# Optimization experiments

Measured on AMD Instinct MI355X. Metric: run time of the kernel, lower is better.

## Reference

```python
import jax, jax.numpy as jnp
import numpy as np

EPS = 1e-6
N_SRC = 100000
N_TAR = 100000
N = N_SRC + N_TAR
DIM = 128
E = 600000
NEG_SLOPE = 0.01  # torch leaky_relu default


def setup_inputs() -> dict:
    key = jax.random.key(0)
    ks = jax.random.split(key, 8)
    x_src = jax.random.normal(ks[0], (N_SRC, DIM), dtype=jnp.float32)
    x_tar = jax.random.normal(ks[1], (N_TAR, DIM), dtype=jnp.float32)
    edge_index = jax.random.randint(ks[2], (2, E), 0, N, dtype=jnp.int64)
    edge_weight = jax.random.uniform(ks[3], (E,), dtype=jnp.float32)
    W_gcn = jax.random.normal(ks[4], (DIM, DIM), dtype=jnp.float32) / np.sqrt(DIM)
    b_gcn = jax.random.normal(ks[5], (DIM,), dtype=jnp.float32) * 0.01
    W_fnn = jax.random.normal(ks[6], (DIM, DIM), dtype=jnp.float32) / np.sqrt(DIM)
    b_fnn = jax.random.normal(ks[7], (DIM,), dtype=jnp.float32) * 0.01
    return dict(x_src=x_src, x_tar=x_tar, edge_index=edge_index,
                edge_weight=edge_weight, W_gcn=W_gcn, b_gcn=b_gcn,
                W_fnn=W_fnn, b_fnn=b_fnn)


def _gcn_conv(x, edge_index, edge_weight, W, b):
    # PyG GCNConv with add_self_loops=True, symmetric normalization.
    row = jnp.concatenate([edge_index[0], jnp.arange(N, dtype=edge_index.dtype)])
    col = jnp.concatenate([edge_index[1], jnp.arange(N, dtype=edge_index.dtype)])
    w = jnp.concatenate([edge_weight, jnp.ones((N,), dtype=edge_weight.dtype)])
    deg = jax.ops.segment_sum(w, col, num_segments=N)
    dinv = jnp.where(deg > 0, jax.lax.rsqrt(deg), 0.0)
    norm = dinv[row] * w * dinv[col]                 # [E+N]
    h = x @ W                                        # [N, D]
    msg = norm[:, None] * h[row]                     # gather + scale
    out = jnp.zeros_like(h).at[col].add(msg)         # scatter-add to targets
    return out + b


def _node_norm(x):
    mean = jnp.mean(x, axis=1, keepdims=True)
    var = jnp.mean((x - mean) ** 2, axis=1, keepdims=True)  # unbiased=False
    return (x - mean) / jnp.sqrt(var + EPS)


def reference(x_src, x_tar, edge_index, edge_weight, W_gcn, b_gcn, W_fnn, b_fnn):
    x = jnp.concatenate([x_src, x_tar], axis=0)      # [N, D]
    # route == 'MIX': GNN branch + FNN branch on the skip copy
    g = _gcn_conv(x, edge_index, edge_weight, W_gcn, b_gcn)
    f = jax.nn.leaky_relu(x @ W_fnn + b_fnn, NEG_SLOPE)  # dropout = identity (eval)
    x = g + f
    x = _node_norm(x)
    x = jax.nn.leaky_relu(x, NEG_SLOPE)
    return x[:N_SRC, :], x[N_SRC:, :]
```

## Files before the change

### kernel.cpp

```cpp
#include <hip/hip_runtime.h>
#include <hip/hip_bf16.h>
#include <cstddef>
#include <cstdint>

#define DIM 128
#define SCAN_CHUNK 2048

typedef __attribute__((ext_vector_type(8))) short short8v;
typedef __attribute__((ext_vector_type(4))) float f32x4;

__device__ __forceinline__ float leaky(float v) {
    return v > 0.0f ? v : 0.01f * v;
}

__device__ __forceinline__ unsigned short f2bf(float f) {
    unsigned u = __builtin_bit_cast(unsigned, f);
    u += 0x7FFF + ((u >> 16) & 1);
    return (unsigned short)(u >> 16);
}

__device__ __forceinline__ unsigned cvt_pk_bf16(float a, float b) {
    unsigned r;
    asm("v_cvt_pk_bf16_f32 %0, %1, %2" : "=v"(r) : "v"(a), "v"(b));
    return r;
}

__device__ __forceinline__ float bf2f_hi(unsigned p) {
    return __builtin_bit_cast(float, p & 0xFFFF0000u);
}
__device__ __forceinline__ float bf2f_lo(unsigned p) {
    return __builtin_bit_cast(float, p << 16);
}

__device__ __forceinline__ void gload_lds16(const float* g, float* lds) {
    __builtin_amdgcn_global_load_lds(
        (const __attribute__((address_space(1))) unsigned int*)g,
        (__attribute__((address_space(3))) unsigned int*)lds, 16, 0, 0);
}

__global__ __launch_bounds__(256)
void init_kernel(const float* __restrict__ Wg, const float* __restrict__ Wf,
                 unsigned short* __restrict__ WgT, unsigned short* __restrict__ WfT,
                 int* __restrict__ cnt, int N) {
    int t = blockIdx.x * 256 + threadIdx.x;
    if (t < N) cnt[t] = 0;
    if (t < 128 * 128) {
        int col = t >> 7, k = t & 127;
        WgT[col * 128 + k] = f2bf(Wg[k * 128 + col]);
        WfT[col * 128 + k] = f2bf(Wf[k * 128 + col]);
    }
}

__global__ __launch_bounds__(256)
void hist_kernel(const int* __restrict__ col, int* __restrict__ cnt, int E) {
    int e = blockIdx.x * blockDim.x + threadIdx.x;
    if (e < E) atomicAdd(&cnt[col[e]], 1);
}

__global__ __launch_bounds__(256)
void scan_block_sums(const int* __restrict__ cnt, int* __restrict__ bsum, int N) {
    __shared__ int sdata[4];
    int base = blockIdx.x * SCAN_CHUNK;
    int s = 0;
    for (int k = threadIdx.x; k < SCAN_CHUNK; k += 256) {
        int idx = base + k;
        s += (idx < N) ? cnt[idx] : 0;
    }
#pragma unroll
    for (int m = 1; m < 64; m <<= 1) s += __shfl_xor(s, m, 64);
    if ((threadIdx.x & 63) == 0) sdata[threadIdx.x >> 6] = s;
    __syncthreads();
    if (threadIdx.x == 0)
        bsum[blockIdx.x] = sdata[0] + sdata[1] + sdata[2] + sdata[3];
}

__global__ __launch_bounds__(128)
void scan_bsum_kernel(int* __restrict__ bsum, int nb) {
    __shared__ int wtot[2];
    int t = threadIdx.x;
    int lane = t & 63;
    int orig = (t < nb) ? bsum[t] : 0;
    int v = orig;
#pragma unroll
    for (int m = 1; m < 64; m <<= 1) {
        int u = __shfl_up(v, m, 64);
        if (lane >= m) v += u;
    }
    if (lane == 63) wtot[t >> 6] = v;
    __syncthreads();
    if (t >= 64) v += wtot[0];
    if (t < nb) bsum[t] = v - orig;
}

__global__ __launch_bounds__(256)
void scan_write_kernel(int* __restrict__ cnt, const int* __restrict__ bsum,
                       int* __restrict__ off, int N) {
    __shared__ int wsum[4];
    int t = threadIdx.x;
    int base = blockIdx.x * SCAN_CHUNK + t * 8;
    int vals[8];
    int local = 0;
#pragma unroll
    for (int k = 0; k < 8; ++k) {
        int idx = base + k;
        int c = (idx < N) ? cnt[idx] : 0;
        vals[k] = local;
        local += c;
    }
    int tsum = local;
    int lane = t & 63;
    int v = tsum;
#pragma unroll
    for (int m = 1; m < 64; m <<= 1) {
        int u = __shfl_up(v, m, 64);
        if (lane >= m) v += u;
    }
    if (lane == 63) wsum[t >> 6] = v;
    __syncthreads();
    int woff = 0;
    for (int i = 0; i < (t >> 6); ++i) woff += wsum[i];
    int texcl = (v - tsum) + woff + bsum[blockIdx.x];
#pragma unroll
    for (int k = 0; k < 8; ++k) {
        int idx = base + k;
        int o = texcl + vals[k];
        if (idx <= N) off[idx] = o;
    }
    __syncthreads();
#pragma unroll
    for (int k = 0; k < 8; ++k) {
        int idx = base + k;
        int o = texcl + vals[k];
        if (idx < N) cnt[idx] = o;
    }
}

__global__ __launch_bounds__(256)
void reorder_kernel(const int* __restrict__ row, const int* __restrict__ col,
                    const float* __restrict__ w, int* __restrict__ cursor,
                    int2* __restrict__ edgeRW, int E) {
    int e = blockIdx.x * blockDim.x + threadIdx.x;
    if (e < E) {
        int c = col[e];
        int pos = atomicAdd(&cursor[c], 1);
        edgeRW[pos] = make_int2(row[e], __builtin_bit_cast(int, w[e]));
    }
}

__global__ __launch_bounds__(256)
void csr_dinv_kernel(const int* __restrict__ off, const int2* __restrict__ edgeRW,
                     float* __restrict__ dinv, int N) {
    int i = blockIdx.x * 256 + threadIdx.x;
    if (i >= N) return;
    int s = off[i], e = off[i + 1];
    float acc = 1.0f;
    for (int j = s; j < e; ++j)
        acc += __builtin_bit_cast(float, edgeRW[j].y);
    dinv[i] = rsqrtf(acc);
}

__global__ __launch_bounds__(512, 4)
void gemm_mfma_kernel(const float* __restrict__ x_src, const float* __restrict__ x_tar,
                      int n_src, int n_total, int ntiles,
                      const unsigned short* __restrict__ WgT,
                      const unsigned short* __restrict__ WfT,
                      const float* __restrict__ bg, const float* __restrict__ bf,
                      const float* __restrict__ dinv,
                      unsigned short* __restrict__ hsb,
                      unsigned short* __restrict__ accb)
{
    __shared__ float Ash[2][64 * 128];

    const int t    = threadIdx.x;
    const int lane = t & 63;
    const int wv   = t >> 6;
    const int h    = wv >> 2;
    const int q    = wv & 3;
    const int lr   = lane & 15;
    const int lk   = lane >> 4;
    const int nb   = gridDim.x;

    short8v wg[4][2], wf[4][2];
#pragma unroll
    for (int ks = 0; ks < 4; ++ks)
#pragma unroll
        for (int nf = 0; nf < 2; ++nf) {
            int col = q * 32 + nf * 16 + lr;
            const size_t bo = (size_t)col * 128 + ks * 32 + lk * 8;
            wg[ks][nf] = *(const short8v*)(WgT + bo);
            wf[ks][nf] = *(const short8v*)(WfT + bo);
        }

    auto stage = [&](int tl, int buf) {
#pragma unroll
        for (int s = 0; s < 4; ++s) {
            int id  = s * 512 + t;
            int row = id >> 5;
            int cs  = id & 31;
            int c   = cs ^ (row & 15);
            int rg  = tl * 64 + row;
            if (rg >= n_total) rg = n_total - 1;
            const float* xr = (rg < n_src) ? x_src + (size_t)rg * DIM
                                           : x_tar + (size_t)(rg - n_src) * DIM;
            gload_lds16(xr + c * 4, &Ash[buf][(size_t)(s * 512 + wv * 64) * 4]);
        }
    };

    int tile = blockIdx.x;
    if (tile < ntiles) stage(tile, 0);
    int cur = 0;

    for (; tile < ntiles; tile += nb) {
        __syncthreads();
        if (tile + nb < ntiles) stage(tile + nb, cur ^ 1);

        f32x4 accg[2][2], accf[2][2];
#pragma unroll
        for (int i = 0; i < 2; ++i)
#pragma unroll
            for (int j = 0; j < 2; ++j) {
                accg[i][j] = (f32x4)0.0f;
                accf[i][j] = (f32x4)0.0f;
            }

#pragma unroll
        for (int ks = 0; ks < 4; ++ks) {
            short8v xf[2];
#pragma unroll
            for (int mf = 0; mf < 2; ++mf) {
                int row = h * 32 + mf * 16 + lr;
                int c0  = ks * 8 + lk * 2;
                float4 q0 = *(const float4*)&Ash[cur][(size_t)(row * 32 + ( c0      ^ (row & 15))) * 4];
                float4 q1 = *(const float4*)&Ash[cur][(size_t)(row * 32 + ((c0 + 1) ^ (row & 15))) * 4];
                union { short8v v; unsigned u[4]; } cv;
                cv.u[0] = cvt_pk_bf16(q0.x, q0.y);
                cv.u[1] = cvt_pk_bf16(q0.z, q0.w);
                cv.u[2] = cvt_pk_bf16(q1.x, q1.y);
                cv.u[3] = cvt_pk_bf16(q1.z, q1.w);
                xf[mf] = cv.v;
            }
#pragma unroll
            for (int nf = 0; nf < 2; ++nf)
#pragma unroll
                for (int mf = 0; mf < 2; ++mf) {
                    accg[mf][nf] = __builtin_amdgcn_mfma_f32_16x16x32_bf16(wg[ks][nf], xf[mf], accg[mf][nf], 0, 0, 0);
                    accf[mf][nf] = __builtin_amdgcn_mfma_f32_16x16x32_bf16(wf[ks][nf], xf[mf], accf[mf][nf], 0, 0, 0);
                }
        }

#pragma unroll
        for (int mf = 0; mf < 2; ++mf) {
            int r = tile * 64 + h * 32 + mf * 16 + lr;
            const bool valid = (r < n_total);
            int rc = valid ? r : (n_total - 1);
            float dv = dinv[rc];
#pragma unroll
            for (int nf = 0; nf < 2; ++nf) {
                int c0 = q * 32 + nf * 16 + lk * 4;
                float4 bgv = *(const float4*)(bg + c0);
                float4 bfv = *(const float4*)(bf + c0);

                float hs0 = dv * accg[mf][nf][0];
                float hs1 = dv * accg[mf][nf][1];
                float hs2 = dv * accg[mf][nf][2];
                float hs3 = dv * accg[mf][nf][3];

                float o0 = leaky(accf[mf][nf][0] + bfv.x) + bgv.x + dv * hs0;
                float o1 = leaky(accf[mf][nf][1] + bfv.y) + bgv.y + dv * hs1;
                float o2 = leaky(accf[mf][nf][2] + bfv.z) + bgv.z + dv * hs2;
                float o3 = leaky(accf[mf][nf][3] + bfv.w) + bgv.w + dv * hs3;

                uint2 hp, op;
                hp.x = cvt_pk_bf16(hs0, hs1);
                hp.y = cvt_pk_bf16(hs2, hs3);
                op.x = cvt_pk_bf16(o0, o1);
                op.y = cvt_pk_bf16(o2, o3);

                if (valid) {
                    *(uint2*)(hsb  + (size_t)r * DIM + c0) = hp;
                    *(uint2*)(accb + (size_t)r * DIM + c0) = op;
                }
            }
        }
        cur ^= 1;
    }
}

__global__ __launch_bounds__(256)
void gather_norm_kernel(const int* __restrict__ off, const int2* __restrict__ edgeRW,
                        const float* __restrict__ dinv,
                        const unsigned short* __restrict__ hsb,
                        const unsigned short* __restrict__ accb,
                        float* __restrict__ out, int n)
{
    const int wid  = threadIdx.x >> 6;
    const int lane = threadIdx.x & 63;
    const int sub  = lane >> 4;
    const int sl   = lane & 15;
    int i = (blockIdx.x * 4 + wid) * 4 + sub;
    if (i >= n) i = n - 1;

    const int start = off[i];
    const int degc  = off[i + 1] - start;

    int md = degc;
    md = max(md, __shfl_xor(md, 16, 64));
    md = max(md, __shfl_xor(md, 32, 64));

    float s[8];
#pragma unroll
    for (int k = 0; k < 8; ++k) s[k] = 0.0f;

    const unsigned short* gbase = hsb + (size_t)sl * 8;

    int   r0 = 0, r1 = 0;
    float w0 = 0.0f, w1 = 0.0f;
    if (0 < degc) { int2 m = edgeRW[start];     r0 = m.x; w0 = __builtin_bit_cast(float, m.y); }
    if (1 < degc) { int2 m = edgeRW[start + 1]; r1 = m.x; w1 = __builtin_bit_cast(float, m.y); }
    uint4 p0 = *(const uint4*)(gbase + (size_t)r0 * DIM);

    for (int t = 0; t < md; ++t) {
        uint4 p1 = p0;
        if (t + 1 < md)
            p1 = *(const uint4*)(gbase + (size_t)r1 * DIM);
        int r2 = 0; float w2 = 0.0f;
        if (t + 2 < md) {
            if (t + 2 < degc) {
                int2 m = edgeRW[start + t + 2];
                r2 = m.x; w2 = __builtin_bit_cast(float, m.y);
            }
        }
        s[0] += w0 * bf2f_lo(p0.x); s[1] += w0 * bf2f_hi(p0.x);
        s[2] += w0 * bf2f_lo(p0.y); s[3] += w0 * bf2f_hi(p0.y);
        s[4] += w0 * bf2f_lo(p0.z); s[5] += w0 * bf2f_hi(p0.z);
        s[6] += w0 * bf2f_lo(p0.w); s[7] += w0 * bf2f_hi(p0.w);
        p0 = p1;
        r0 = r1; w0 = w1;
        r1 = r2; w1 = w2;
    }

    const float dv = dinv[i];
    uint4 av = *(const uint4*)(accb + (size_t)i * DIM + sl * 8);
    float v[8];
    v[0] = bf2f_lo(av.x) + dv * s[0]; v[1] = bf2f_hi(av.x) + dv * s[1];
    v[2] = bf2f_lo(av.y) + dv * s[2]; v[3] = bf2f_hi(av.y) + dv * s[3];
    v[4] = bf2f_lo(av.z) + dv * s[4]; v[5] = bf2f_hi(av.z) + dv * s[5];
    v[6] = bf2f_lo(av.w) + dv * s[6]; v[7] = bf2f_hi(av.w) + dv * s[7];

    float sum = 0.0f;
#pragma unroll
    for (int k = 0; k < 8; ++k) sum += v[k];
#pragma unroll
    for (int m = 1; m < 16; m <<= 1) sum += __shfl_xor(sum, m, 64);
    const float mean = sum * (1.0f / 128.0f);

    float sq = 0.0f;
#pragma unroll
    for (int k = 0; k < 8; ++k) {
        v[k] -= mean;
        sq += v[k] * v[k];
    }
#pragma unroll
    for (int m = 1; m < 16; m <<= 1) sq += __shfl_xor(sq, m, 64);
    const float rstd = rsqrtf(sq * (1.0f / 128.0f) + 1e-6f);

    float4 o1, o2;
    o1.x = leaky(v[0] * rstd); o1.y = leaky(v[1] * rstd);
    o1.z = leaky(v[2] * rstd); o1.w = leaky(v[3] * rstd);
    o2.x = leaky(v[4] * rstd); o2.y = leaky(v[5] * rstd);
    o2.z = leaky(v[6] * rstd); o2.w = leaky(v[7] * rstd);
    float* op = out + (size_t)i * DIM + sl * 8;
    *(float4*)op       = o1;
    *(float4*)(op + 4) = o2;
}

extern "C" void kernel_launch(void* const* d_in, const int* in_sizes, int n_in,
                              void* d_out, int out_size, void* d_ws, size_t ws_size,
                              hipStream_t stream)
{
    const float* x_src = (const float*)d_in[0];
    const float* x_tar = (const float*)d_in[1];
    const int*   ei    = (const int*)d_in[2];
    const float* ew    = (const float*)d_in[3];
    const float* Wg    = (const float*)d_in[4];
    const float* bg    = (const float*)d_in[5];
    const float* Wf    = (const float*)d_in[6];
    const float* bf    = (const float*)d_in[7];

    const int n_src = in_sizes[0] / DIM;
    const int n_tar = in_sizes[1] / DIM;
    const int N     = n_src + n_tar;
    const int E     = in_sizes[3];

    const int* rowp = ei;
    const int* colp = ei + E;

    char* p = (char*)d_ws;
    float* dinv = (float*)p;  p += (size_t)N * 4;
    int*   cnt  = (int*)p;    p += (size_t)N * 4;
    int*   off  = (int*)p;    p += (size_t)(N + 1) * 4;
    int*   bsum = (int*)p;    p += 160 * 4;
    p = (char*)(((uintptr_t)p + 15) & ~(uintptr_t)15);
    int2*  edgeRW = (int2*)p; p += (size_t)E * 8;
    unsigned short* hsb  = (unsigned short*)p; p += (size_t)N * DIM * 2;
    unsigned short* accb = (unsigned short*)p; p += (size_t)N * DIM * 2;
    unsigned short* WgT  = (unsigned short*)p; p += 128 * 128 * 2;
    unsigned short* WfT  = (unsigned short*)p;

    const int NB = (N + 1 + SCAN_CHUNK - 1) / SCAN_CHUNK;

    init_kernel<<<(N + 255) / 256, 256, 0, stream>>>(Wg, Wf, WgT, WfT, cnt, N);

    hist_kernel<<<(E + 255) / 256, 256, 0, stream>>>(colp, cnt, E);

    scan_block_sums<<<NB, 256, 0, stream>>>(cnt, bsum, N);
    scan_bsum_kernel<<<1, 128, 0, stream>>>(bsum, NB);
    scan_write_kernel<<<NB, 256, 0, stream>>>(cnt, bsum, off, N);

    reorder_kernel<<<(E + 255) / 256, 256, 0, stream>>>(rowp, colp, ew, cnt,
                                                        edgeRW, E);

    csr_dinv_kernel<<<(N + 255) / 256, 256, 0, stream>>>(off, edgeRW, dinv, N);

    const int ntiles = (N + 63) / 64;
    gemm_mfma_kernel<<<512, 512, 0, stream>>>(
        x_src, x_tar, n_src, N, ntiles, WgT, WfT, bg, bf, dinv, hsb, accb);

    gather_norm_kernel<<<(N + 15) / 16, 256, 0, stream>>>(
        off, edgeRW, dinv, hsb, accb, (float*)d_out, N);
}
```

Baseline: 226.2 us.

## Deepen GEMM staging pipeline to four 32-row buffers with contiguous tile ranges

The fused dual-GEMM kernel now uses 32-row tiles with a four-slot LDS ring that keeps three tiles in flight, instead of a two-slot double buffer of 64-row tiles. Each block takes a contiguous range of tiles. It waits on hand-tuned vmcnt values rather than a full drain, so loads overlap compute more deeply. dinv values for the block's rows are preloaded into shared memory, and biases are hoisted out of the loop. The hand-counted vmcnt thresholds are fragile, and halving the tile height halves the MFMA work per barrier.

```diff
diff --git a/kernel.cpp b/kernel.cpp
--- a/kernel.cpp
+++ b/kernel.cpp
@@ -169,7 +169,8 @@
                       unsigned short* __restrict__ hsb,
                       unsigned short* __restrict__ accb)
 {
-    __shared__ float Ash[2][64 * 128];
+    __shared__ float Ash[4][32 * 128];
+    __shared__ float dinvS[448];
 
     const int t    = threadIdx.x;
     const int lane = t & 63;
@@ -178,7 +179,19 @@
     const int q    = wv & 3;
     const int lr   = lane & 15;
     const int lk   = lane >> 4;
-    const int nb   = gridDim.x;
+
+    const int nb  = gridDim.x;
+    const int K   = (ntiles + nb - 1) / nb;
+    const int t0  = blockIdx.x * K;
+    const int cnt = min(K, ntiles - t0);
+    if (cnt <= 0) return;
+
+    if (t < cnt * 32) {
+        int gi = t0 * 32 + t;
+        if (gi >= n_total) gi = n_total - 1;
+        dinvS[t] = dinv[gi];
+    }
+    asm volatile("s_waitcnt lgkmcnt(0)" ::: "memory");
 
     short8v wg[4][2], wf[4][2];
 #pragma unroll
@@ -190,15 +203,22 @@
             wg[ks][nf] = *(const short8v*)(WgT + bo);
             wf[ks][nf] = *(const short8v*)(WfT + bo);
         }
+    float4 bgv[2], bfv[2];
+#pragma unroll
+    for (int nf = 0; nf < 2; ++nf) {
+        int c0 = q * 32 + nf * 16 + lk * 4;
+        bgv[nf] = *(const float4*)(bg + c0);
+        bfv[nf] = *(const float4*)(bf + c0);
+    }
 
     auto stage = [&](int tl, int buf) {
 #pragma unroll
-        for (int s = 0; s < 4; ++s) {
+        for (int s = 0; s < 2; ++s) {
             int id  = s * 512 + t;
             int row = id >> 5;
             int cs  = id & 31;
             int c   = cs ^ (row & 15);
-            int rg  = tl * 64 + row;
+            int rg  = tl * 32 + row;
             if (rg >= n_total) rg = n_total - 1;
             const float* xr = (rg < n_src) ? x_src + (size_t)rg * DIM
                                            : x_tar + (size_t)(rg - n_src) * DIM;
@@ -206,83 +226,81 @@
         }
     };
 
-    int tile = blockIdx.x;
-    if (tile < ntiles) stage(tile, 0);
-    int cur = 0;
-
-    for (; tile < ntiles; tile += nb) {
-        __syncthreads();
-        if (tile + nb < ntiles) stage(tile + nb, cur ^ 1);
-
-        f32x4 accg[2][2], accf[2][2];
-#pragma unroll
-        for (int i = 0; i < 2; ++i)
-#pragma unroll
-            for (int j = 0; j < 2; ++j) {
-                accg[i][j] = (f32x4)0.0f;
-                accf[i][j] = (f32x4)0.0f;
+    stage(t0, 0);
+    if (1 < cnt) stage(t0 + 1, 1);
+    if (2 < cnt) stage(t0 + 2, 2);
+
+    const int xrow = h * 16 + lr;
+    const int xrs  = xrow & 15;
+
+    for (int it = 0; it < cnt; ++it) {
+        if (cnt >= 6) {
+            if (it == 0)              asm volatile("s_waitcnt vmcnt(4)"  ::: "memory");
+            else if (it == 1)         asm volatile("s_waitcnt vmcnt(8)"  ::: "memory");
+            else if (it == 2)         asm volatile("s_waitcnt vmcnt(12)" ::: "memory");
+            else if (it == cnt - 2)   asm volatile("s_waitcnt vmcnt(14)" ::: "memory");
+            else if (it == cnt - 1)   asm volatile("s_waitcnt vmcnt(12)" ::: "memory");
+            else                      asm volatile("s_waitcnt vmcnt(16)" ::: "memory");
+        } else {
+            asm volatile("s_waitcnt vmcnt(0)" ::: "memory");
+        }
+        __builtin_amdgcn_sched_barrier(0);
+        __builtin_amdgcn_s_barrier();
+        __builtin_amdgcn_sched_barrier(0);
+
+        if (it + 3 < cnt) stage(t0 + it + 3, (it + 3) & 3);
+
+        const int cur = it & 3;
+        f32x4 accg[2], accf[2];
+        accg[0] = (f32x4)0.0f; accg[1] = (f32x4)0.0f;
+        accf[0] = (f32x4)0.0f; accf[1] = (f32x4)0.0f;
+
+#pragma unroll
+        for (int ks = 0; ks < 4; ++ks) {
+            int c0 = ks * 8 + lk * 2;
+            float4 q0 = *(const float4*)&Ash[cur][(size_t)(xrow * 32 + ( c0      ^ xrs)) * 4];
+            float4 q1 = *(const float4*)&Ash[cur][(size_t)(xrow * 32 + ((c0 + 1) ^ xrs)) * 4];
+            union { short8v v; unsigned u[4]; } cv;
+            cv.u[0] = cvt_pk_bf16(q0.x, q0.y);
+            cv.u[1] = cvt_pk_bf16(q0.z, q0.w);
+            cv.u[2] = cvt_pk_bf16(q1.x, q1.y);
+            cv.u[3] = cvt_pk_bf16(q1.z, q1.w);
+#pragma unroll
+            for (int nf = 0; nf < 2; ++nf) {
+                accg[nf] = __builtin_amdgcn_mfma_f32_16x16x32_bf16(wg[ks][nf], cv.v, accg[nf], 0, 0, 0);
+                accf[nf] = __builtin_amdgcn_mfma_f32_16x16x32_bf16(wf[ks][nf], cv.v, accf[nf], 0, 0, 0);
             }
-
-#pragma unroll
-        for (int ks = 0; ks < 4; ++ks) {
-            short8v xf[2];
-#pragma unroll
-            for (int mf = 0; mf < 2; ++mf) {
-                int row = h * 32 + mf * 16 + lr;
-                int c0  = ks * 8 + lk * 2;
-                float4 q0 = *(const float4*)&Ash[cur][(size_t)(row * 32 + ( c0      ^ (row & 15))) * 4];
-                float4 q1 = *(const float4*)&Ash[cur][(size_t)(row * 32 + ((c0 + 1) ^ (row & 15))) * 4];
-                union { short8v v; unsigned u[4]; } cv;
-                cv.u[0] = cvt_pk_bf16(q0.x, q0.y);
-                cv.u[1] = cvt_pk_bf16(q0.z, q0.w);
-                cv.u[2] = cvt_pk_bf16(q1.x, q1.y);
-                cv.u[3] = cvt_pk_bf16(q1.z, q1.w);
-                xf[mf] = cv.v;
+        }
+
+        const int tile = t0 + it;
+        int r = tile * 32 + xrow;
+        const bool valid = (r < n_total);
+        float dv = dinvS[it * 32 + xrow];
+#pragma unroll
+        for (int nf = 0; nf < 2; ++nf) {
+            int c0 = q * 32 + nf * 16 + lk * 4;
+
+            float hs0 = dv * accg[nf][0];
+            float hs1 = dv * accg[nf][1];
+            float hs2 = dv * accg[nf][2];
+            float hs3 = dv * accg[nf][3];
+
+            float o0 = leaky(accf[nf][0] + bfv[nf].x) + bgv[nf].x + dv * hs0;
+            float o1 = leaky(accf[nf][1] + bfv[nf].y) + bgv[nf].y + dv * hs1;
+            float o2 = leaky(accf[nf][2] + bfv[nf].z) + bgv[nf].z + dv * hs2;
+            float o3 = leaky(accf[nf][3] + bfv[nf].w) + bgv[nf].w + dv * hs3;
+
+            uint2 hp, op;
+            hp.x = cvt_pk_bf16(hs0, hs1);
+            hp.y = cvt_pk_bf16(hs2, hs3);
+            op.x = cvt_pk_bf16(o0, o1);
+            op.y = cvt_pk_bf16(o2, o3);
+
+            if (valid) {
+                *(uint2*)(hsb  + (size_t)r * DIM + c0) = hp;
+                *(uint2*)(accb + (size_t)r * DIM + c0) = op;
             }
-#pragma unroll
-            for (int nf = 0; nf < 2; ++nf)
-#pragma unroll
-                for (int mf = 0; mf < 2; ++mf) {
-                    accg[mf][nf] = __builtin_amdgcn_mfma_f32_16x16x32_bf16(wg[ks][nf], xf[mf], accg[mf][nf], 0, 0, 0);
-                    accf[mf][nf] = __builtin_amdgcn_mfma_f32_16x16x32_bf16(wf[ks][nf], xf[mf], accf[mf][nf], 0, 0, 0);
-                }
-        }
-
-#pragma unroll
-        for (int mf = 0; mf < 2; ++mf) {
-            int r = tile * 64 + h * 32 + mf * 16 + lr;
-            const bool valid = (r < n_total);
-            int rc = valid ? r : (n_total - 1);
-            float dv = dinv[rc];
-#pragma unroll
-            for (int nf = 0; nf < 2; ++nf) {
-                int c0 = q * 32 + nf * 16 + lk * 4;
-                float4 bgv = *(const float4*)(bg + c0);
-                float4 bfv = *(const float4*)(bf + c0);
-
-                float hs0 = dv * accg[mf][nf][0];
-                float hs1 = dv * accg[mf][nf][1];
-                float hs2 = dv * accg[mf][nf][2];
-                float hs3 = dv * accg[mf][nf][3];
-
-                float o0 = leaky(accf[mf][nf][0] + bfv.x) + bgv.x + dv * hs0;
-                float o1 = leaky(accf[mf][nf][1] + bfv.y) + bgv.y + dv * hs1;
-                float o2 = leaky(accf[mf][nf][2] + bfv.z) + bgv.z + dv * hs2;
-                float o3 = leaky(accf[mf][nf][3] + bfv.w) + bgv.w + dv * hs3;
-
-                uint2 hp, op;
-                hp.x = cvt_pk_bf16(hs0, hs1);
-                hp.y = cvt_pk_bf16(hs2, hs3);
-                op.x = cvt_pk_bf16(o0, o1);
-                op.y = cvt_pk_bf16(o2, o3);
-
-                if (valid) {
-                    *(uint2*)(hsb  + (size_t)r * DIM + c0) = hp;
-                    *(uint2*)(accb + (size_t)r * DIM + c0) = op;
-                }
-            }
-        }
-        cur ^= 1;
+        }
     }
 }
 
@@ -422,7 +440,7 @@
 
     csr_dinv_kernel<<<(N + 255) / 256, 256, 0, stream>>>(off, edgeRW, dinv, N);
 
-    const int ntiles = (N + 63) / 64;
+    const int ntiles = (N + 31) / 32;
     gemm_mfma_kernel<<<512, 512, 0, stream>>>(
         x_src, x_tar, n_src, N, ntiles, WgT, WfT, bg, bf, dinv, hsb, accb);
 
```

Result: faster. 205.6 us (-9.1%).

## Replace LDS-staged persistent GEMM with direct-load one-tile-per-block GEMM

Applied to the files above, without the earlier changes.

Rewrites the dual-weight MFMA GEMM so each 256-thread block handles 32 rows and loads x straight from global memory into registers, dropping the double-buffered LDS staging, the persistent tile loop and its barriers. The weight column mapping is permuted so each lane owns 8 contiguous output columns, which allows 16-byte bf16 stores instead of 8-byte ones. This removes LDS traffic and synchronisation, at the cost of losing load/compute overlap and having each x row read by all four waves, with the repeat reads served from cache.

```diff
diff --git a/kernel.cpp b/kernel.cpp
--- a/kernel.cpp
+++ b/kernel.cpp
@@ -30,12 +30,6 @@
 }
 __device__ __forceinline__ float bf2f_lo(unsigned p) {
     return __builtin_bit_cast(float, p << 16);
-}
-
-__device__ __forceinline__ void gload_lds16(const float* g, float* lds) {
-    __builtin_amdgcn_global_load_lds(
-        (const __attribute__((address_space(1))) unsigned int*)g,
-        (__attribute__((address_space(3))) unsigned int*)lds, 16, 0, 0);
 }
 
 __global__ __launch_bounds__(256)
@@ -159,130 +153,107 @@
     dinv[i] = rsqrtf(acc);
 }
 
-__global__ __launch_bounds__(512, 4)
-void gemm_mfma_kernel(const float* __restrict__ x_src, const float* __restrict__ x_tar,
-                      int n_src, int n_total, int ntiles,
-                      const unsigned short* __restrict__ WgT,
-                      const unsigned short* __restrict__ WfT,
-                      const float* __restrict__ bg, const float* __restrict__ bf,
-                      const float* __restrict__ dinv,
-                      unsigned short* __restrict__ hsb,
-                      unsigned short* __restrict__ accb)
+__global__ __launch_bounds__(256, 3)
+void gemm_direct_kernel(const float* __restrict__ x_src, const float* __restrict__ x_tar,
+                        int n_src, int n_total,
+                        const unsigned short* __restrict__ WgT,
+                        const unsigned short* __restrict__ WfT,
+                        const float* __restrict__ bg, const float* __restrict__ bf,
+                        const float* __restrict__ dinv,
+                        unsigned short* __restrict__ hsb,
+                        unsigned short* __restrict__ accb)
 {
-    __shared__ float Ash[2][64 * 128];
-
     const int t    = threadIdx.x;
     const int lane = t & 63;
-    const int wv   = t >> 6;
-    const int h    = wv >> 2;
-    const int q    = wv & 3;
+    const int q    = t >> 6;
     const int lr   = lane & 15;
     const int lk   = lane >> 4;
-    const int nb   = gridDim.x;
 
     short8v wg[4][2], wf[4][2];
 #pragma unroll
     for (int ks = 0; ks < 4; ++ks)
 #pragma unroll
         for (int nf = 0; nf < 2; ++nf) {
-            int col = q * 32 + nf * 16 + lr;
+            int col = q * 32 + ((lr >> 2) << 3) + nf * 4 + (lr & 3);
             const size_t bo = (size_t)col * 128 + ks * 32 + lk * 8;
             wg[ks][nf] = *(const short8v*)(WgT + bo);
             wf[ks][nf] = *(const short8v*)(WfT + bo);
         }
-
-    auto stage = [&](int tl, int buf) {
-#pragma unroll
-        for (int s = 0; s < 4; ++s) {
-            int id  = s * 512 + t;
-            int row = id >> 5;
-            int cs  = id & 31;
-            int c   = cs ^ (row & 15);
-            int rg  = tl * 64 + row;
-            if (rg >= n_total) rg = n_total - 1;
-            const float* xr = (rg < n_src) ? x_src + (size_t)rg * DIM
-                                           : x_tar + (size_t)(rg - n_src) * DIM;
-            gload_lds16(xr + c * 4, &Ash[buf][(size_t)(s * 512 + wv * 64) * 4]);
+    const int cb = q * 32 + lk * 8;
+    float4 bgv[2], bfv[2];
+#pragma unroll
+    for (int nf = 0; nf < 2; ++nf) {
+        bgv[nf] = *(const float4*)(bg + cb + nf * 4);
+        bfv[nf] = *(const float4*)(bf + cb + nf * 4);
+    }
+
+    const int rowbase = blockIdx.x * 32;
+    const float* xr[2];
+    int   rr[2];
+    bool  vld[2];
+    float dv[2];
+#pragma unroll
+    for (int mf = 0; mf < 2; ++mf) {
+        int r = rowbase + mf * 16 + lr;
+        vld[mf] = (r < n_total);
+        int rc = vld[mf] ? r : (n_total - 1);
+        rr[mf] = r;
+        xr[mf] = (rc < n_src) ? x_src + (size_t)rc * DIM
+                              : x_tar + (size_t)(rc - n_src) * DIM;
+        dv[mf] = dinv[rc];
+    }
+
+    f32x4 accg[2][2], accf[2][2];
+#pragma unroll
+    for (int i = 0; i < 2; ++i)
+#pragma unroll
+        for (int j = 0; j < 2; ++j) {
+            accg[i][j] = (f32x4)0.0f;
+            accf[i][j] = (f32x4)0.0f;
         }
-    };
-
-    int tile = blockIdx.x;
-    if (tile < ntiles) stage(tile, 0);
-    int cur = 0;
-
-    for (; tile < ntiles; tile += nb) {
-        __syncthreads();
-        if (tile + nb < ntiles) stage(tile + nb, cur ^ 1);
-
-        f32x4 accg[2][2], accf[2][2];
-#pragma unroll
-        for (int i = 0; i < 2; ++i)
-#pragma unroll
-            for (int j = 0; j < 2; ++j) {
-                accg[i][j] = (f32x4)0.0f;
-                accf[i][j] = (f32x4)0.0f;
-            }
-
-#pragma unroll
-        for (int ks = 0; ks < 4; ++ks) {
-            short8v xf[2];
-#pragma unroll
-            for (int mf = 0; mf < 2; ++mf) {
-                int row = h * 32 + mf * 16 + lr;
-                int c0  = ks * 8 + lk * 2;
-                float4 q0 = *(const float4*)&Ash[cur][(size_t)(row * 32 + ( c0      ^ (row & 15))) * 4];
-                float4 q1 = *(const float4*)&Ash[cur][(size_t)(row * 32 + ((c0 + 1) ^ (row & 15))) * 4];
-                union { short8v v; unsigned u[4]; } cv;
-                cv.u[0] = cvt_pk_bf16(q0.x, q0.y);
-                cv.u[1] = cvt_pk_bf16(q0.z, q0.w);
-                cv.u[2] = cvt_pk_bf16(q1.x, q1.y);
-                cv.u[3] = cvt_pk_bf16(q1.z, q1.w);
-                xf[mf] = cv.v;
-            }
-#pragma unroll
-            for (int nf = 0; nf < 2; ++nf)
-#pragma unroll
-                for (int mf = 0; mf < 2; ++mf) {
-                    accg[mf][nf] = __builtin_amdgcn_mfma_f32_16x16x32_bf16(wg[ks][nf], xf[mf], accg[mf][nf], 0, 0, 0);
-                    accf[mf][nf] = __builtin_amdgcn_mfma_f32_16x16x32_bf16(wf[ks][nf], xf[mf], accf[mf][nf], 0, 0, 0);
-                }
-        }
-
+
+#pragma unroll
+    for (int ks = 0; ks < 4; ++ks) {
 #pragma unroll
         for (int mf = 0; mf < 2; ++mf) {
-            int r = tile * 64 + h * 32 + mf * 16 + lr;
-            const bool valid = (r < n_total);
-            int rc = valid ? r : (n_total - 1);
-            float dv = dinv[rc];
+            float4 q0 = *(const float4*)(xr[mf] + ks * 32 + lk * 8);
+            float4 q1 = *(const float4*)(xr[mf] + ks * 32 + lk * 8 + 4);
+            union { short8v v; unsigned u[4]; } cv;
+            cv.u[0] = cvt_pk_bf16(q0.x, q0.y);
+            cv.u[1] = cvt_pk_bf16(q0.z, q0.w);
+            cv.u[2] = cvt_pk_bf16(q1.x, q1.y);
+            cv.u[3] = cvt_pk_bf16(q1.z, q1.w);
 #pragma unroll
             for (int nf = 0; nf < 2; ++nf) {
-                int c0 = q * 32 + nf * 16 + lk * 4;
-                float4 bgv = *(const float4*)(bg + c0);
-                float4 bfv = *(const float4*)(bf + c0);
-
-                float hs0 = dv * accg[mf][nf][0];
-                float hs1 = dv * accg[mf][nf][1];
-                float hs2 = dv * accg[mf][nf][2];
-                float hs3 = dv * accg[mf][nf][3];
-
-                float o0 = leaky(accf[mf][nf][0] + bfv.x) + bgv.x + dv * hs0;
-                float o1 = leaky(accf[mf][nf][1] + bfv.y) + bgv.y + dv * hs1;
-                float o2 = leaky(accf[mf][nf][2] + bfv.z) + bgv.z + dv * hs2;
-                float o3 = leaky(accf[mf][nf][3] + bfv.w) + bgv.w + dv * hs3;
-
-                uint2 hp, op;
-                hp.x = cvt_pk_bf16(hs0, hs1);
-                hp.y = cvt_pk_bf16(hs2, hs3);
-                op.x = cvt_pk_bf16(o0, o1);
-                op.y = cvt_pk_bf16(o2, o3);
-
-                if (valid) {
-                    *(uint2*)(hsb  + (size_t)r * DIM + c0) = hp;
-                    *(uint2*)(accb + (size_t)r * DIM + c0) = op;
-                }
+                accg[mf][nf] = __builtin_amdgcn_mfma_f32_16x16x32_bf16(wg[ks][nf], cv.v, accg[mf][nf], 0, 0, 0);
+                accf[mf][nf] = __builtin_amdgcn_mfma_f32_16x16x32_bf16(wf[ks][nf], cv.v, accf[mf][nf], 0, 0, 0);
             }
         }
-        cur ^= 1;
+    }
+
+#pragma unroll
+    for (int mf = 0; mf < 2; ++mf) {
+        float hs[8], oo[8];
+#pragma unroll
+        for (int nf = 0; nf < 2; ++nf)
+#pragma unroll
+            for (int e = 0; e < 4; ++e) {
+                int k = nf * 4 + e;
+                hs[k] = dv[mf] * accg[mf][nf][e];
+                float f = accf[mf][nf][e] + ((const float*)&bfv[nf])[e];
+                oo[k] = leaky(f) + ((const float*)&bgv[nf])[e] + dv[mf] * hs[k];
+            }
+
+        uint4 hp, op;
+        hp.x = cvt_pk_bf16(hs[0], hs[1]); hp.y = cvt_pk_bf16(hs[2], hs[3]);
+        hp.z = cvt_pk_bf16(hs[4], hs[5]); hp.w = cvt_pk_bf16(hs[6], hs[7]);
+        op.x = cvt_pk_bf16(oo[0], oo[1]); op.y = cvt_pk_bf16(oo[2], oo[3]);
+        op.z = cvt_pk_bf16(oo[4], oo[5]); op.w = cvt_pk_bf16(oo[6], oo[7]);
+
+        if (vld[mf]) {
+            *(uint4*)(hsb  + (size_t)rr[mf] * DIM + cb) = hp;
+            *(uint4*)(accb + (size_t)rr[mf] * DIM + cb) = op;
+        }
     }
 }
 
@@ -422,9 +393,8 @@
 
     csr_dinv_kernel<<<(N + 255) / 256, 256, 0, stream>>>(off, edgeRW, dinv, N);
 
-    const int ntiles = (N + 63) / 64;
-    gemm_mfma_kernel<<<512, 512, 0, stream>>>(
-        x_src, x_tar, n_src, N, ntiles, WgT, WfT, bg, bf, dinv, hsb, accb);
+    gemm_direct_kernel<<<(N + 31) / 32, 256, 0, stream>>>(
+        x_src, x_tar, n_src, N, WgT, WfT, bg, bf, dinv, hsb, accb);
 
     gather_norm_kernel<<<(N + 15) / 16, 256, 0, stream>>>(
         off, edgeRW, dinv, hsb, accb, (float*)d_out, N);
```

Result: slower. 266.4 us (+17.8%).
